# Optimization experiments

Hardware: AMD Instinct MI355X
Metric: run time of the kernel (lower is better)

Reference implementation:

```python
import jax, jax.numpy as jnp
import numpy as np
import math

B_, V_, D_, N_, H_, W_ = 4, 8, 64, 16, 32, 32
V_LIST = [0.0, 45.0, 90.0, 135.0, 180.0, 225.0, 270.0, 315.0]
GROUPS = 4
EPS = 1e-5


def _make_sample_coords():
    # Replicates F.affine_grid(align_corners=False) for fixed rotation matrices,
    # then maps normalized grid coords to input pixel coords as grid_sample does.
    xs = (np.arange(W_) + 0.5) * 2.0 / W_ - 1.0
    ys = (np.arange(H_) + 0.5) * 2.0 / H_ - 1.0
    X, Y = np.meshgrid(xs, ys)  # (H, W)
    ix_list, iy_list = [], []
    for w in V_LIST:
        a = math.radians(-w)
        c, s = math.cos(a), math.sin(a)
        gx = c * X - s * Y  # theta = [[c,-s,0],[s,c,0]]
        gy = s * X + c * Y
        ix_list.append((gx + 1.0) * W_ / 2.0 - 0.5)
        iy_list.append((gy + 1.0) * H_ / 2.0 - 0.5)
    return (jnp.asarray(np.stack(ix_list), jnp.float32),
            jnp.asarray(np.stack(iy_list), jnp.float32))

IX, IY = _make_sample_coords()  # each (V, H, W)


def _bilinear(sv, iy, ix):
    # sv: (B, D, N, H, W); iy, ix: (H, W) float sampling coords (pixel space)
    x0 = jnp.floor(ix)
    y0 = jnp.floor(iy)
    wx1 = ix - x0
    wy1 = iy - y0

    def corner(yc, xc, wgt):
        m = (yc >= 0) & (yc < H_) & (xc >= 0) & (xc < W_)  # zeros padding
        yi = jnp.clip(yc, 0, H_ - 1).astype(jnp.int32)
        xi = jnp.clip(xc, 0, W_ - 1).astype(jnp.int32)
        return sv[..., yi, xi] * jnp.where(m, wgt, 0.0)

    return (corner(y0, x0, (1.0 - wy1) * (1.0 - wx1))
            + corner(y0, x0 + 1.0, (1.0 - wy1) * wx1)
            + corner(y0 + 1.0, x0, wy1 * (1.0 - wx1))
            + corner(y0 + 1.0, x0 + 1.0, wy1 * wx1))

# vmap over the velocity axis V of s_prev and the per-velocity grids
_transport = jax.vmap(_bilinear, in_axes=(1, 0, 0), out_axes=1)


def _conv(x, w, b=None):
    y = jax.lax.conv_general_dilated(x, w, (1, 1), 'SAME',
                                     dimension_numbers=('NCHW', 'OIHW', 'NCHW'))
    if b is not None:
        y = y + b[None, :, None, None]
    return y


def _group_norm(x, w, b):
    Bn, D, H, W = x.shape
    xg = x.reshape(Bn, GROUPS, D // GROUPS, H, W)
    mu = xg.mean(axis=(2, 3, 4), keepdims=True)
    var = xg.var(axis=(2, 3, 4), keepdims=True)
    xn = ((xg - mu) * jax.lax.rsqrt(var + EPS)).reshape(Bn, D, H, W)
    return xn * w[None, :, None, None] + b[None, :, None, None]


def setup_inputs() -> dict:
    key = jax.random.key(0)
    ks = jax.random.split(key, 5)
    return {
        "u_t": jax.random.normal(ks[0], (B_, D_, H_, W_), jnp.float32),
        "s_prev": jax.random.normal(ks[1], (B_, V_, D_, N_, H_, W_), jnp.float32) * 0.1,
        "gn_w": jnp.ones((D_,), jnp.float32),
        "gn_b": jnp.zeros((D_,), jnp.float32),
        "conv_delta_w": jax.random.normal(ks[2], (D_, D_, 3, 3), jnp.float32) * 0.02,
        "conv_delta_b": jnp.zeros((D_,), jnp.float32),
        "conv_B_w": jax.random.normal(ks[3], (N_, D_, 3, 3), jnp.float32) * 0.02,
        "conv_C_w": jax.random.normal(ks[4], (N_, D_, 3, 3), jnp.float32) * 0.02,
        "log_A_real": jnp.full((D_, N_), math.log(0.5), jnp.float32),
        "D_param": jnp.ones((D_,), jnp.float32),
        "dt_bias": jnp.float32(math.log(math.e - 1.0)),
    }


def reference(u_t, s_prev, gn_w, gn_b, conv_delta_w, conv_delta_b,
              conv_B_w, conv_C_w, log_A_real, D_param, dt_bias):
    u_norm = _group_norm(u_t, gn_w, gn_b)
    delta = jax.nn.softplus(_conv(u_norm, conv_delta_w, conv_delta_b) + dt_bias)
    delta = jnp.clip(delta, 1e-4, 5.0)                               # (B,D,H,W)
    B_val = _conv(u_norm, conv_B_w)                                  # (B,N,H,W)
    C_val = _conv(u_norm, conv_C_w)                                  # (B,N,H,W)
    A = -jnp.exp(log_A_real)                                         # (D,N)
    A_bar = jnp.exp(delta[:, :, None] * A[None, :, :, None, None])   # (B,D,N,H,W)
    B_bar = delta[:, :, None] * B_val[:, None]                       # (B,D,N,H,W)
    s_trans = _transport(s_prev, IY, IX)                             # (B,V,D,N,H,W)
    s_new = A_bar[:, None] * s_trans + B_bar[:, None] * u_t[:, None, :, None]
    y_state = jnp.einsum('bvdnhw,bnhw->bvdhw', s_new, C_val)
    y_new = y_state + u_t[:, None] * D_param[None, None, :, None, None]
    return (y_new, s_new)
```

## Files before the change

kernel.cpp:

```cpp
#include <hip/hip_runtime.h>
#include <cmath>

#define FSQ 0.70710678118654752440f
__constant__ float CTAB[8] = {1.f,  FSQ, 0.f, -FSQ, -1.f, -FSQ, 0.f, FSQ};
__constant__ float STAB[8] = {0.f, -FSQ, -1.f, -FSQ,  0.f,  FSQ, 1.f, FSQ};

typedef float f4 __attribute__((ext_vector_type(4)));

__global__ __launch_bounds__(1024) void gn_kernel(const float* __restrict__ u,
                                                  const float* __restrict__ gw,
                                                  const float* __restrict__ gb,
                                                  float* __restrict__ up)
{
    int blk = blockIdx.x;
    int b = blk >> 2, g = blk & 3;
    int t = threadIdx.x;
    const float* src = u + ((size_t)(b * 64 + g * 16) << 10);
    float sum = 0.f, sq = 0.f;
    #pragma unroll
    for (int r = 0; r < 16; ++r) {
        float v = src[t + (r << 10)];
        sum += v; sq += v * v;
    }
    #pragma unroll
    for (int ofs = 32; ofs > 0; ofs >>= 1) {
        sum += __shfl_down(sum, ofs);
        sq  += __shfl_down(sq, ofs);
    }
    __shared__ float red[16], red2[16];
    int wv = t >> 6;
    if ((t & 63) == 0) { red[wv] = sum; red2[wv] = sq; }
    __syncthreads();
    float s_tot = 0.f, q_tot = 0.f;
    #pragma unroll
    for (int k = 0; k < 16; ++k) { s_tot += red[k]; q_tot += red2[k]; }
    float mu  = s_tot * (1.f / 16384.f);
    float var = q_tot * (1.f / 16384.f) - mu * mu;
    float rs  = rsqrtf(var + 1e-5f);

    float* pb = up + (size_t)(b * 64 + g * 16) * 1156;
    for (int k = t; k < 16 * 132; k += 1024) {
        int pl = k / 132, c = k - pl * 132;
        int idx;
        if (c < 34)       idx = c;
        else if (c < 68)  idx = 33 * 34 + (c - 34);
        else if (c < 100) idx = (c - 68 + 1) * 34;
        else              idx = (c - 100 + 1) * 34 + 33;
        pb[pl * 1156 + idx] = 0.f;
    }
    int y = t >> 5, x = t & 31;
    #pragma unroll
    for (int r = 0; r < 16; ++r) {
        float val = (src[t + (r << 10)] - mu) * rs * gw[g * 16 + r] + gb[g * 16 + r];
        pb[r * 1156 + (y + 1) * 34 + (x + 1)] = val;
    }
}

__global__ __launch_bounds__(256) void conv_kernel(const float* __restrict__ up,
                                                   const float* __restrict__ wd,
                                                   const float* __restrict__ bd,
                                                   const float* __restrict__ wB,
                                                   const float* __restrict__ wC,
                                                   const float* __restrict__ dtb,
                                                   float* __restrict__ delta,
                                                   float* __restrict__ Bv,
                                                   float* __restrict__ Cv)
{
    __shared__ float sin_[64 * 204];
    int blk = blockIdx.x;
    int strip = blk & 7;
    int og = (blk >> 3) % 24;
    int b = blk / 192;
    int h0 = strip * 4;
    int t = threadIdx.x;

    const float* plane = up + (size_t)b * 73984;
    for (int idx = t; idx < 13056; idx += 256) {
        int ci = idx / 204;
        int rem = idx - ci * 204;
        sin_[idx] = plane[ci * 1156 + h0 * 34 + rem];
    }
    __syncthreads();

    int o0 = og * 4;
    const float* wsel;
    if (o0 < 64)      wsel = wd + (size_t)o0 * 576;
    else if (o0 < 80) wsel = wB + (size_t)(o0 - 64) * 576;
    else              wsel = wC + (size_t)(o0 - 80) * 576;

    int half = t >> 7;
    int px = t & 127;
    int r = px >> 5, c = px & 31;
    const float* base = sin_ + r * 34 + c;

    float acc0 = 0.f, acc1 = 0.f, acc2 = 0.f, acc3 = 0.f;
    int ci0 = half * 32;
    for (int ci = ci0; ci < ci0 + 32; ++ci) {
        const float* pp = base + ci * 204;
        const float* wp = wsel + ci * 9;
        #pragma unroll
        for (int dy = 0; dy < 3; ++dy)
            #pragma unroll
            for (int dx = 0; dx < 3; ++dx) {
                float v = pp[dy * 34 + dx];
                int wi = dy * 3 + dx;
                acc0 += v * wp[wi];
                acc1 += v * wp[576 + wi];
                acc2 += v * wp[1152 + wi];
                acc3 += v * wp[1728 + wi];
            }
    }
    __syncthreads();
    float4* red4 = (float4*)sin_;
    red4[t] = make_float4(acc0, acc1, acc2, acc3);
    __syncthreads();
    if (t < 128) {
        float4 a = red4[t], bq = red4[t + 128];
        float s0 = a.x + bq.x, s1 = a.y + bq.y, s2 = a.z + bq.z, s3 = a.w + bq.w;
        float s[4] = {s0, s1, s2, s3};
        int pidx = (h0 + r) * 32 + c;
        if (o0 < 64) {
            #pragma unroll
            for (int k = 0; k < 4; ++k) {
                float x = s[k] + bd[o0 + k] + dtb[0];
                float sp = (x > 20.f) ? x : log1pf(expf(x));
                sp = fminf(fmaxf(sp, 1e-4f), 5.f);
                delta[((size_t)(b * 64 + o0 + k) << 10) + pidx] = sp;
            }
        } else if (o0 < 80) {
            #pragma unroll
            for (int k = 0; k < 4; ++k)
                Bv[((size_t)(b * 16 + o0 - 64 + k) << 10) + pidx] = s[k];
        } else {
            #pragma unroll
            for (int k = 0; k < 4; ++k)
                Cv[((size_t)(b * 16 + o0 - 80 + k) << 10) + pidx] = s[k];
        }
    }
}

__global__ __launch_bounds__(256) void fused_state_kernel(
    const float* __restrict__ s_prev, const float* __restrict__ u_t,
    const float* __restrict__ delta, const float* __restrict__ Bv,
    const float* __restrict__ Cv, const float* __restrict__ logA,
    const float* __restrict__ Dp, float* __restrict__ y_out,
    float* __restrict__ s_out)
{
    __shared__ float lds[4 * 1190];
    __shared__ float Ash[16];
    int blk = blockIdx.x;
    int d = blk & 63, v = (blk >> 6) & 7, b = blk >> 9;
    int t = threadIdx.x;

    if (t < 16) Ash[t] = -__expf(logA[d * 16 + t]);
    for (int k = t; k < 528; k += 256) {
        int pl = k / 132, g = k - pl * 132;
        int idx;
        if (g < 34)       idx = g;
        else if (g < 68)  idx = 33 * 35 + (g - 34);
        else if (g < 100) idx = (g - 67) * 35;
        else              idx = (g - 99) * 35 + 33;
        lds[pl * 1190 + idx] = 0.f;
    }

    size_t so_base = ((size_t)((b * 8 + v) * 64 + d)) << 14;
    const float cc = CTAB[v], ss = STAB[v];
    const f4* dpl4 = (const f4*)(delta + ((size_t)(b * 64 + d) << 10));
    const f4* upl4 = (const f4*)(u_t   + ((size_t)(b * 64 + d) << 10));
    float Dd = Dp[d];

    f4 dd4 = dpl4[t], uv4 = upl4[t];

    int h = t >> 3;
    float Yc = (h + 0.5f) * 0.0625f - 1.f;
    float w00[4], w01[4], w10[4], w11[4], duv[4], yacc[4];
    int tb[4];
    #pragma unroll
    for (int j = 0; j < 4; ++j) {
        int wpx = ((t & 7) << 2) | j;
        float X = (wpx + 0.5f) * 0.0625f - 1.f;
        float gx = cc * X - ss * Yc;
        float gy = ss * X + cc * Yc;
        float ix = (gx + 1.f) * 16.f - 0.5f;
        float iy = (gy + 1.f) * 16.f - 0.5f;
        float fx0 = floorf(ix), fy0 = floorf(iy);
        float wx = ix - fx0, wy = iy - fy0;
        int x0 = (int)fx0, y0 = (int)fy0;
        float mx0 = (x0 >= 0 && x0 < 32) ? (1.f - wx) : 0.f;
        float mx1 = (x0 >= -1 && x0 < 31) ? wx : 0.f;
        float my0 = (y0 >= 0 && y0 < 32) ? (1.f - wy) : 0.f;
        float my1 = (y0 >= -1 && y0 < 31) ? wy : 0.f;
        w00[j] = my0 * mx0; w01[j] = my0 * mx1;
        w10[j] = my1 * mx0; w11[j] = my1 * mx1;
        int bx = min(max(x0, -1), 31), by = min(max(y0, -1), 31);
        tb[j] = (by + 1) * 35 + (bx + 1);
        duv[j] = dd4[j] * uv4[j];
        yacc[j] = 0.f;
    }

    #pragma unroll 1
    for (int c = 0; c < 4; ++c) {
        if (c) __syncthreads();
        const float4* src = (const float4*)(s_prev + so_base + ((size_t)c << 12));
        #pragma unroll
        for (int k = 0; k < 4; ++k) {
            int q = t + (k << 8);
            float4 val = src[q];
            int lin = q << 2;
            int nn = lin >> 10, rem = lin & 1023;
            int di = nn * 1190 + ((rem >> 5) + 1) * 35 + (rem & 31) + 1;
            lds[di] = val.x; lds[di + 1] = val.y; lds[di + 2] = val.z; lds[di + 3] = val.w;
        }
        __syncthreads();

        const f4* bvc4 = (const f4*)(Bv + ((size_t)b << 14) + (c << 12));
        const f4* cvc4 = (const f4*)(Cv + ((size_t)b << 14) + (c << 12));
        f4* soc4 = (f4*)(s_out + so_base + ((size_t)c << 12));
        #pragma unroll
        for (int nn = 0; nn < 4; ++nn) {
            f4 B4 = bvc4[(nn << 8) + t];
            f4 C4 = cvc4[(nn << 8) + t];
            float An = Ash[(c << 2) + nn];
            f4 sn4;
            #pragma unroll
            for (int j = 0; j < 4; ++j) {
                int si = tb[j] + nn * 1190;
                float bil = lds[si] * w00[j] + lds[si + 1] * w01[j]
                          + lds[si + 35] * w10[j] + lds[si + 36] * w11[j];
                float abar = __expf(dd4[j] * An);
                float sn = abar * bil + duv[j] * B4[j];
                sn4[j] = sn;
                yacc[j] += sn * C4[j];
            }
            soc4[(nn << 8) + t] = sn4;
        }
    }

    f4 y4;
    #pragma unroll
    for (int j = 0; j < 4; ++j) y4[j] = yacc[j] + uv4[j] * Dd;
    f4* yo4 = (f4*)(y_out + (((size_t)((b * 8 + v) * 64 + d)) << 10));
    yo4[t] = y4;
}

extern "C" void kernel_launch(void* const* d_in, const int* in_sizes, int n_in,
                              void* d_out, int out_size, void* d_ws, size_t ws_size,
                              hipStream_t stream)
{
    const float* u_t    = (const float*)d_in[0];
    const float* s_prev = (const float*)d_in[1];
    const float* gn_w   = (const float*)d_in[2];
    const float* gn_b   = (const float*)d_in[3];
    const float* wd     = (const float*)d_in[4];
    const float* bd     = (const float*)d_in[5];
    const float* wB     = (const float*)d_in[6];
    const float* wC     = (const float*)d_in[7];
    const float* logA   = (const float*)d_in[8];
    const float* Dp     = (const float*)d_in[9];
    const float* dtb    = (const float*)d_in[10];

    float* y_out = (float*)d_out;
    float* s_out = y_out + 2097152;

    float* up    = (float*)d_ws;
    float* delta = up + 295936;
    float* Bv    = delta + 262144;
    float* Cv    = Bv + 65536;

    hipLaunchKernelGGL(gn_kernel, dim3(16), dim3(1024), 0, stream, u_t, gn_w, gn_b, up);
    hipLaunchKernelGGL(conv_kernel, dim3(768), dim3(256), 0, stream,
                       up, wd, bd, wB, wC, dtb, delta, Bv, Cv);
    hipLaunchKernelGGL(fused_state_kernel, dim3(2048), dim3(256), 0, stream,
                       s_prev, u_t, delta, Bv, Cv, logA, Dp, y_out, s_out);
}
```

Measured before the change: 306.1 us.

## Double-buffer s_prev chunks in LDS and vectorize conv input staging

The fused state kernel now keeps two LDS buffers and prefetches the next chunk of s_prev into registers while the current chunk is computed, then writes it to the alternate buffer. This replaces the load-then-sync-then-compute pattern, which exposed global load latency on every chunk. The conv kernel's shared-memory staging loop is also changed to use float4 loads. The cost is double the LDS footprint, which may lower occupancy, and more live registers for the prefetched data.

```diff
diff --git a/kernel.cpp b/kernel.cpp
--- a/kernel.cpp
+++ b/kernel.cpp
@@ -74,11 +74,15 @@
     int h0 = strip * 4;
     int t = threadIdx.x;
 
-    const float* plane = up + (size_t)b * 73984;
-    for (int idx = t; idx < 13056; idx += 256) {
-        int ci = idx / 204;
-        int rem = idx - ci * 204;
-        sin_[idx] = plane[ci * 1156 + h0 * 34 + rem];
+    const float4* plane4 = (const float4*)(up + (size_t)b * 73984 + h0 * 34);
+    float4* s4 = (float4*)sin_;
+    #pragma unroll
+    for (int k = 0; k < 13; ++k) {
+        int i4 = t + (k << 8);
+        if (i4 < 3264) {
+            int ci = i4 / 51, r4 = i4 - ci * 51;
+            s4[i4] = plane4[ci * 289 + r4];
+        }
     }
     __syncthreads();
 
@@ -146,14 +150,14 @@
     const float* __restrict__ Dp, float* __restrict__ y_out,
     float* __restrict__ s_out)
 {
-    __shared__ float lds[4 * 1190];
+    __shared__ float lds[2 * 4 * 1190];
     __shared__ float Ash[16];
     int blk = blockIdx.x;
     int d = blk & 63, v = (blk >> 6) & 7, b = blk >> 9;
     int t = threadIdx.x;
 
     if (t < 16) Ash[t] = -__expf(logA[d * 16 + t]);
-    for (int k = t; k < 528; k += 256) {
+    for (int k = t; k < 1056; k += 256) {
         int pl = k / 132, g = k - pl * 132;
         int idx;
         if (g < 34)       idx = g;
@@ -164,6 +168,17 @@
     }
 
     size_t so_base = ((size_t)((b * 8 + v) * 64 + d)) << 14;
+    const float4* src = (const float4*)(s_prev + so_base);
+
+#define DSW(nb, q, val) { int lin = (q) << 2; int nn = lin >> 10; int rem = lin & 1023; \
+    int di = (nb) + nn * 1190 + ((rem >> 5) + 1) * 35 + (rem & 31) + 1; \
+    lds[di] = (val).x; lds[di + 1] = (val).y; lds[di + 2] = (val).z; lds[di + 3] = (val).w; }
+
+    {
+        float4 a0 = src[t], a1 = src[t + 256], a2 = src[t + 512], a3 = src[t + 768];
+        DSW(0, t, a0); DSW(0, t + 256, a1); DSW(0, t + 512, a2); DSW(0, t + 768, a3);
+    }
+
     const float cc = CTAB[v], ss = STAB[v];
     const f4* dpl4 = (const f4*)(delta + ((size_t)(b * 64 + d) << 10));
     const f4* upl4 = (const f4*)(u_t   + ((size_t)(b * 64 + d) << 10));
@@ -197,21 +212,18 @@
         duv[j] = dd4[j] * uv4[j];
         yacc[j] = 0.f;
     }
+    __syncthreads();
 
     #pragma unroll 1
     for (int c = 0; c < 4; ++c) {
-        if (c) __syncthreads();
-        const float4* src = (const float4*)(s_prev + so_base + ((size_t)c << 12));
-        #pragma unroll
-        for (int k = 0; k < 4; ++k) {
-            int q = t + (k << 8);
-            float4 val = src[q];
-            int lin = q << 2;
-            int nn = lin >> 10, rem = lin & 1023;
-            int di = nn * 1190 + ((rem >> 5) + 1) * 35 + (rem & 31) + 1;
-            lds[di] = val.x; lds[di + 1] = val.y; lds[di + 2] = val.z; lds[di + 3] = val.w;
-        }
-        __syncthreads();
+        int cb = (c & 1) * 4760;
+        float4 r0, r1, r2, r3;
+        if (c < 3) {
+            int o = (c + 1) << 10;
+            r0 = src[o + t];       r1 = src[o + t + 256];
+            r2 = src[o + t + 512]; r3 = src[o + t + 768];
+            asm volatile("" ::: "memory");
+        }
 
         const f4* bvc4 = (const f4*)(Bv + ((size_t)b << 14) + (c << 12));
         const f4* cvc4 = (const f4*)(Cv + ((size_t)b << 14) + (c << 12));
@@ -224,7 +236,7 @@
             f4 sn4;
             #pragma unroll
             for (int j = 0; j < 4; ++j) {
-                int si = tb[j] + nn * 1190;
+                int si = cb + tb[j] + nn * 1190;
                 float bil = lds[si] * w00[j] + lds[si + 1] * w01[j]
                           + lds[si + 35] * w10[j] + lds[si + 36] * w11[j];
                 float abar = __expf(dd4[j] * An);
@@ -234,7 +246,15 @@
             }
             soc4[(nn << 8) + t] = sn4;
         }
-    }
+
+        if (c < 3) {
+            int nb = cb ^ 4760;
+            DSW(nb, t, r0); DSW(nb, t + 256, r1);
+            DSW(nb, t + 512, r2); DSW(nb, t + 768, r3);
+        }
+        __syncthreads();
+    }
+#undef DSW
 
     f4 y4;
     #pragma unroll
```

Result: no change. 300.2 us (-1.9%).

## Specialize state transport for axis-aligned rotations as exact pixel permutations

Applied to the files above, without the earlier changes.

The fused state kernel now branches on the velocity angle. At 0° and 180° it reads s_prev directly from global memory, identity or reversed, with no LDS staging. At 90° and 270° it uses an unpadded LDS transpose with a 33-float stride in place of bilinear interpolation. Only the diagonal angles keep the padded-LDS bilinear path. The conv kernel's input staging is also vectorized to float4 loads. This relies on the sample coordinates for multiples of 90° landing exactly on integer pixels, and it adds block-level divergence across kernel variants.

```diff
diff --git a/kernel.cpp b/kernel.cpp
--- a/kernel.cpp
+++ b/kernel.cpp
@@ -74,11 +74,15 @@
     int h0 = strip * 4;
     int t = threadIdx.x;
 
-    const float* plane = up + (size_t)b * 73984;
-    for (int idx = t; idx < 13056; idx += 256) {
-        int ci = idx / 204;
-        int rem = idx - ci * 204;
-        sin_[idx] = plane[ci * 1156 + h0 * 34 + rem];
+    const float4* plane4 = (const float4*)(up + (size_t)b * 73984 + h0 * 34);
+    float4* s4 = (float4*)sin_;
+    #pragma unroll
+    for (int k = 0; k < 13; ++k) {
+        int i4 = t + (k << 8);
+        if (i4 < 3264) {
+            int ci = i4 / 51, r4 = i4 - ci * 51;
+            s4[i4] = plane4[ci * 289 + r4];
+        }
     }
     __syncthreads();
 
@@ -116,8 +120,7 @@
     __syncthreads();
     if (t < 128) {
         float4 a = red4[t], bq = red4[t + 128];
-        float s0 = a.x + bq.x, s1 = a.y + bq.y, s2 = a.z + bq.z, s3 = a.w + bq.w;
-        float s[4] = {s0, s1, s2, s3};
+        float s[4] = {a.x + bq.x, a.y + bq.y, a.z + bq.z, a.w + bq.w};
         int pidx = (h0 + r) * 32 + c;
         if (o0 < 64) {
             #pragma unroll
@@ -153,86 +156,160 @@
     int t = threadIdx.x;
 
     if (t < 16) Ash[t] = -__expf(logA[d * 16 + t]);
-    for (int k = t; k < 528; k += 256) {
-        int pl = k / 132, g = k - pl * 132;
-        int idx;
-        if (g < 34)       idx = g;
-        else if (g < 68)  idx = 33 * 35 + (g - 34);
-        else if (g < 100) idx = (g - 67) * 35;
-        else              idx = (g - 99) * 35 + 33;
-        lds[pl * 1190 + idx] = 0.f;
-    }
 
     size_t so_base = ((size_t)((b * 8 + v) * 64 + d)) << 14;
-    const float cc = CTAB[v], ss = STAB[v];
+    const f4* src4 = (const f4*)(s_prev + so_base);
     const f4* dpl4 = (const f4*)(delta + ((size_t)(b * 64 + d) << 10));
     const f4* upl4 = (const f4*)(u_t   + ((size_t)(b * 64 + d) << 10));
+    const f4* bvb  = (const f4*)(Bv + ((size_t)b << 14));
+    const f4* cvb  = (const f4*)(Cv + ((size_t)b << 14));
+    f4* soc4 = (f4*)(s_out + so_base);
     float Dd = Dp[d];
 
     f4 dd4 = dpl4[t], uv4 = upl4[t];
-
-    int h = t >> 3;
-    float Yc = (h + 0.5f) * 0.0625f - 1.f;
-    float w00[4], w01[4], w10[4], w11[4], duv[4], yacc[4];
-    int tb[4];
-    #pragma unroll
-    for (int j = 0; j < 4; ++j) {
-        int wpx = ((t & 7) << 2) | j;
-        float X = (wpx + 0.5f) * 0.0625f - 1.f;
-        float gx = cc * X - ss * Yc;
-        float gy = ss * X + cc * Yc;
-        float ix = (gx + 1.f) * 16.f - 0.5f;
-        float iy = (gy + 1.f) * 16.f - 0.5f;
-        float fx0 = floorf(ix), fy0 = floorf(iy);
-        float wx = ix - fx0, wy = iy - fy0;
-        int x0 = (int)fx0, y0 = (int)fy0;
-        float mx0 = (x0 >= 0 && x0 < 32) ? (1.f - wx) : 0.f;
-        float mx1 = (x0 >= -1 && x0 < 31) ? wx : 0.f;
-        float my0 = (y0 >= 0 && y0 < 32) ? (1.f - wy) : 0.f;
-        float my1 = (y0 >= -1 && y0 < 31) ? wy : 0.f;
-        w00[j] = my0 * mx0; w01[j] = my0 * mx1;
-        w10[j] = my1 * mx0; w11[j] = my1 * mx1;
-        int bx = min(max(x0, -1), 31), by = min(max(y0, -1), 31);
-        tb[j] = (by + 1) * 35 + (bx + 1);
-        duv[j] = dd4[j] * uv4[j];
-        yacc[j] = 0.f;
-    }
-
-    #pragma unroll 1
-    for (int c = 0; c < 4; ++c) {
-        if (c) __syncthreads();
-        const float4* src = (const float4*)(s_prev + so_base + ((size_t)c << 12));
+    int h = t >> 3, x0 = (t & 7) << 2;
+    f4 duv, yacc;
+    #pragma unroll
+    for (int j = 0; j < 4; ++j) { duv[j] = dd4[j] * uv4[j]; yacc[j] = 0.f; }
+
+    if (v == 0) {
+        __syncthreads();
+        #pragma unroll 4
+        for (int pl = 0; pl < 16; ++pl) {
+            int idx = (pl << 8) + t;
+            f4 sp = src4[idx];
+            f4 B4 = bvb[idx], C4 = cvb[idx];
+            float An = Ash[pl];
+            f4 sn4;
+            #pragma unroll
+            for (int j = 0; j < 4; ++j) {
+                float sn = __expf(dd4[j] * An) * sp[j] + duv[j] * B4[j];
+                sn4[j] = sn; yacc[j] += sn * C4[j];
+            }
+            soc4[idx] = sn4;
+        }
+    } else if (v == 4) {
+        __syncthreads();
+        int tin = ((31 - h) << 3) + (7 - (t & 7));
+        #pragma unroll 4
+        for (int pl = 0; pl < 16; ++pl) {
+            int idx = (pl << 8) + t;
+            f4 sp = src4[(pl << 8) + tin];
+            f4 B4 = bvb[idx], C4 = cvb[idx];
+            float An = Ash[pl];
+            f4 sn4;
+            #pragma unroll
+            for (int j = 0; j < 4; ++j) {
+                float sn = __expf(dd4[j] * An) * sp[3 - j] + duv[j] * B4[j];
+                sn4[j] = sn; yacc[j] += sn * C4[j];
+            }
+            soc4[idx] = sn4;
+        }
+    } else if (!(v & 1)) {
+        int pb2 = (31 - x0) * 33 + h;
+        int pb6 = x0 * 33 + (31 - h);
+        #pragma unroll 1
+        for (int c = 0; c < 4; ++c) {
+            if (c) __syncthreads();
+            const float4* srcc = (const float4*)(s_prev + so_base + ((size_t)c << 12));
+            #pragma unroll
+            for (int k = 0; k < 4; ++k) {
+                int q = t + (k << 8);
+                float4 val = srcc[q];
+                int lin = q << 2;
+                int nn = lin >> 10, rem = lin & 1023;
+                int di = nn * 1056 + ((rem >> 5) * 33) + (rem & 31);
+                lds[di] = val.x; lds[di + 1] = val.y; lds[di + 2] = val.z; lds[di + 3] = val.w;
+            }
+            __syncthreads();
+            #pragma unroll
+            for (int nn = 0; nn < 4; ++nn) {
+                int idx = (((c << 2) + nn) << 8) + t;
+                f4 B4 = bvb[idx], C4 = cvb[idx];
+                float An = Ash[(c << 2) + nn];
+                f4 sn4;
+                if (v == 2) {
+                    #pragma unroll
+                    for (int j = 0; j < 4; ++j) {
+                        float sp = lds[nn * 1056 + pb2 - j * 33];
+                        float sn = __expf(dd4[j] * An) * sp + duv[j] * B4[j];
+                        sn4[j] = sn; yacc[j] += sn * C4[j];
+                    }
+                } else {
+                    #pragma unroll
+                    for (int j = 0; j < 4; ++j) {
+                        float sp = lds[nn * 1056 + pb6 + j * 33];
+                        float sn = __expf(dd4[j] * An) * sp + duv[j] * B4[j];
+                        sn4[j] = sn; yacc[j] += sn * C4[j];
+                    }
+                }
+                soc4[idx] = sn4;
+            }
+        }
+    } else {
+        for (int k = t; k < 528; k += 256) {
+            int pl = k / 132, g = k - pl * 132;
+            int idx;
+            if (g < 34)       idx = g;
+            else if (g < 68)  idx = 33 * 35 + (g - 34);
+            else if (g < 100) idx = (g - 67) * 35;
+            else              idx = (g - 99) * 35 + 33;
+            lds[pl * 1190 + idx] = 0.f;
+        }
+        const float cc = CTAB[v], ss = STAB[v];
+        float Yc = (h + 0.5f) * 0.0625f - 1.f;
+        float w00[4], w01[4], w10[4], w11[4];
+        int tb[4];
         #pragma unroll
-        for (int k = 0; k < 4; ++k) {
-            int q = t + (k << 8);
-            float4 val = src[q];
-            int lin = q << 2;
-            int nn = lin >> 10, rem = lin & 1023;
-            int di = nn * 1190 + ((rem >> 5) + 1) * 35 + (rem & 31) + 1;
-            lds[di] = val.x; lds[di + 1] = val.y; lds[di + 2] = val.z; lds[di + 3] = val.w;
-        }
-        __syncthreads();
-
-        const f4* bvc4 = (const f4*)(Bv + ((size_t)b << 14) + (c << 12));
-        const f4* cvc4 = (const f4*)(Cv + ((size_t)b << 14) + (c << 12));
-        f4* soc4 = (f4*)(s_out + so_base + ((size_t)c << 12));
-        #pragma unroll
-        for (int nn = 0; nn < 4; ++nn) {
-            f4 B4 = bvc4[(nn << 8) + t];
-            f4 C4 = cvc4[(nn << 8) + t];
-            float An = Ash[(c << 2) + nn];
-            f4 sn4;
-            #pragma unroll
-            for (int j = 0; j < 4; ++j) {
-                int si = tb[j] + nn * 1190;
-                float bil = lds[si] * w00[j] + lds[si + 1] * w01[j]
-                          + lds[si + 35] * w10[j] + lds[si + 36] * w11[j];
-                float abar = __expf(dd4[j] * An);
-                float sn = abar * bil + duv[j] * B4[j];
-                sn4[j] = sn;
-                yacc[j] += sn * C4[j];
-            }
-            soc4[(nn << 8) + t] = sn4;
+        for (int j = 0; j < 4; ++j) {
+            int wpx = x0 | j;
+            float X = (wpx + 0.5f) * 0.0625f - 1.f;
+            float gx = cc * X - ss * Yc;
+            float gy = ss * X + cc * Yc;
+            float ix = (gx + 1.f) * 16.f - 0.5f;
+            float iy = (gy + 1.f) * 16.f - 0.5f;
+            float fx0 = floorf(ix), fy0 = floorf(iy);
+            float wx = ix - fx0, wy = iy - fy0;
+            int xx0 = (int)fx0, yy0 = (int)fy0;
+            float mx0 = (xx0 >= 0 && xx0 < 32) ? (1.f - wx) : 0.f;
+            float mx1 = (xx0 >= -1 && xx0 < 31) ? wx : 0.f;
+            float my0 = (yy0 >= 0 && yy0 < 32) ? (1.f - wy) : 0.f;
+            float my1 = (yy0 >= -1 && yy0 < 31) ? wy : 0.f;
+            w00[j] = my0 * mx0; w01[j] = my0 * mx1;
+            w10[j] = my1 * mx0; w11[j] = my1 * mx1;
+            int bx = min(max(xx0, -1), 31), by = min(max(yy0, -1), 31);
+            tb[j] = (by + 1) * 35 + (bx + 1);
+        }
+        #pragma unroll 1
+        for (int c = 0; c < 4; ++c) {
+            if (c) __syncthreads();
+            const float4* srcc = (const float4*)(s_prev + so_base + ((size_t)c << 12));
+            #pragma unroll
+            for (int k = 0; k < 4; ++k) {
+                int q = t + (k << 8);
+                float4 val = srcc[q];
+                int lin = q << 2;
+                int nn = lin >> 10, rem = lin & 1023;
+                int di = nn * 1190 + ((rem >> 5) + 1) * 35 + (rem & 31) + 1;
+                lds[di] = val.x; lds[di + 1] = val.y; lds[di + 2] = val.z; lds[di + 3] = val.w;
+            }
+            __syncthreads();
+            #pragma unroll
+            for (int nn = 0; nn < 4; ++nn) {
+                int idx = (((c << 2) + nn) << 8) + t;
+                f4 B4 = bvb[idx], C4 = cvb[idx];
+                float An = Ash[(c << 2) + nn];
+                f4 sn4;
+                #pragma unroll
+                for (int j = 0; j < 4; ++j) {
+                    int si = tb[j] + nn * 1190;
+                    float bil = lds[si] * w00[j] + lds[si + 1] * w01[j]
+                              + lds[si + 35] * w10[j] + lds[si + 36] * w11[j];
+                    float sn = __expf(dd4[j] * An) * bil + duv[j] * B4[j];
+                    sn4[j] = sn; yacc[j] += sn * C4[j];
+                }
+                soc4[idx] = sn4;
+            }
         }
     }
 
```

Result: slower. 319.0 us (+4.2%).
